# Kernel tuning notes

Measured on AMD Instinct MI355X. Metric: run time of the kernel, lower is better.

The kernel has to match this reference:

```python
import jax, jax.numpy as jnp
import numpy as np

B, T, HID = 1, 2048, 2048
H, KVH, D = 32, 8, 64
G = H // KVH          # kv groups = 4
SCALE = 1.0 / np.sqrt(D)
NEG = -1e9


def _rotate_half(x):
    x1, x2 = x[..., : D // 2], x[..., D // 2 :]
    return jnp.concatenate((-x2, x1), axis=-1)


def setup_inputs() -> dict:
    key = jax.random.key(0)
    ks = jax.random.split(key, 8)
    hidden_states = jax.random.normal(ks[0], (B, T, HID), jnp.float32)
    # RoPE tables (faithful shapes; realistic values)
    pos = jnp.arange(T, dtype=jnp.float32)[:, None]
    inv = 1.0 / (10000.0 ** (jnp.arange(0, D, 2, dtype=jnp.float32) / D))
    ang = pos * inv[None, :]                      # [T, D/2]
    ang = jnp.concatenate([ang, ang], axis=-1)    # [T, D]
    cos = jnp.broadcast_to(jnp.cos(ang)[None], (B, T, D))
    sin = jnp.broadcast_to(jnp.sin(ang)[None], (B, T, D))
    # causal additive mask [B,1,T,T]
    causal = jnp.tril(jnp.ones((T, T), bool))
    attention_mask_4d = jnp.where(causal, 0.0, NEG).astype(jnp.float32)[None, None]
    s = 0.02
    Wq = jax.random.normal(ks[1], (H * D, HID), jnp.float32) * s
    Wk = jax.random.normal(ks[2], (KVH * D, HID), jnp.float32) * s
    Wv = jax.random.normal(ks[3], (KVH * D, HID), jnp.float32) * s
    Wo = jax.random.normal(ks[4], (HID, H * D), jnp.float32) * s
    return {"hidden_states": hidden_states, "cos": cos, "sin": sin,
            "attention_mask_4d": attention_mask_4d,
            "Wq": Wq, "Wk": Wk, "Wv": Wv, "Wo": Wo}


def reference(hidden_states, cos, sin, attention_mask_4d, Wq, Wk, Wv, Wo):
    x = hidden_states
    b, t, _ = x.shape
    # QKV projections (nn.Linear: x @ W.T), then [B, heads, T, D]
    q = (x @ Wq.T).reshape(b, t, H, D).transpose(0, 2, 1, 3)
    k = (x @ Wk.T).reshape(b, t, KVH, D).transpose(0, 2, 1, 3)
    v = (x @ Wv.T).reshape(b, t, KVH, D).transpose(0, 2, 1, 3)
    # rotary: cos/sin [B,T,D] -> broadcast over heads
    c = cos[:, None]; s = sin[:, None]
    q = q * c + _rotate_half(q) * s
    k = k * c + _rotate_half(k) * s
    # grouped-query attention with fp32 scores/softmax
    qg = q.reshape(b, KVH, G, t, D)
    scores = jnp.einsum('bkgtd,bksd->bkgts', qg.astype(jnp.float32),
                        k.astype(jnp.float32)) * SCALE
    m = attention_mask_4d[:, 0].astype(jnp.float32)  # [B,T,S]
    scores = scores + m[:, None, None, :, :]
    probs = jax.nn.softmax(scores, axis=-1)
    out = jnp.einsum('bkgts,bksd->bkgtd', probs.astype(v.dtype), v)
    out = out.astype(q.dtype).reshape(b, H, t, D)
    out = out.transpose(0, 2, 1, 3).reshape(b, t, H * D)
    return out @ Wo.T
```

## Files before the change

### kernel.cpp

```cpp
#include <hip/hip_runtime.h>
#include <math.h>

typedef __attribute__((ext_vector_type(8))) __bf16 bf16x8;
typedef __attribute__((ext_vector_type(4))) float  f32x4;
typedef unsigned short ushort_t;
typedef unsigned int   uint_t;

static __device__ inline f32x4 mfma16(bf16x8 a, bf16x8 b, f32x4 c) {
    return __builtin_amdgcn_mfma_f32_16x16x32_bf16(a, b, c, 0, 0, 0);
}

static __device__ inline ushort_t f2b(float f) {
    uint_t u = __builtin_bit_cast(uint_t, f);
    u = (u + 0x7FFFu + ((u >> 16) & 1u)) >> 16;
    return (ushort_t)u;
}
static __device__ inline float b2f(ushort_t u) {
    uint_t x = ((uint_t)u) << 16;
    return __builtin_bit_cast(float, x);
}
static __device__ inline bf16x8 ld8(const ushort_t* p) {
    uint4 v = *(const uint4*)p;
    return __builtin_bit_cast(bf16x8, v);
}
static __device__ inline float fexp2(float x) {
#if __has_builtin(__builtin_amdgcn_exp2f)
    return __builtin_amdgcn_exp2f(x);
#else
    return exp2f(x);
#endif
}

static __device__ inline void gl_lds16(const ushort_t* g, ushort_t* l) {
    __builtin_amdgcn_global_load_lds(
        (const __attribute__((address_space(1))) void*)(g),
        (__attribute__((address_space(3))) void*)(l),
        16, 0, 0);
}

#define WS_XB     0
#define WS_WQKV   8388608
#define WS_WO     20971520
#define WS_P0     29360128
#define WS_P1     41943040
#define WS_QBB    0
#define WS_KBB    8388608
#define WS_VTG    10485760
#define WS_AB     12582912
#define WS_O0     29360128
#define WS_O1     46137344

__global__ __launch_bounds__(256) void cvt_all(const float* __restrict__ x,
                                               const float* __restrict__ wq,
                                               const float* __restrict__ wk,
                                               const float* __restrict__ wv,
                                               const float* __restrict__ wo,
                                               ushort_t* __restrict__ dst) {
    const size_t i = (size_t)(blockIdx.x * 256 + threadIdx.x) * 4;
    const float* src; size_t off;
    if (i < 4194304)       { src = x;  off = 0; }
    else if (i < 8388608)  { src = wq; off = 4194304; }
    else if (i < 9437184)  { src = wk; off = 8388608; }
    else if (i < 10485760) { src = wv; off = 9437184; }
    else                   { src = wo; off = 10485760; }
    float4 v = *(const float4*)(src + (i - off));
    ushort4 o;
    o.x = f2b(v.x); o.y = f2b(v.y); o.z = f2b(v.z); o.w = f2b(v.w);
    *(ushort4*)(dst + i) = o;
}

template <int OUTB>
__global__ __launch_bounds__(512, 2) void gemm256(const ushort_t* __restrict__ A,
                                                  const ushort_t* __restrict__ Bt,
                                                  void* __restrict__ C0,
                                                  void* __restrict__ C1,
                                                  int N, int K) {
    __shared__ ushort_t lds[65536];
    const int tid  = threadIdx.x;
    const int lane = tid & 63, w = tid >> 6;
    const int qn = lane & 15, quad = lane >> 4;
    const long m0 = (long)blockIdx.y * 256;
    const long n0 = (long)blockIdx.x * 256;
    const int kh   = K >> 1;
    const int kbeg = blockIdx.z * kh;
    const int NT   = kh >> 6;
    void* Cout = blockIdx.z ? C1 : C0;
    ushort_t* ldsp = lds;

    const int srow = w * 8 + (lane >> 3);
    const int scol = ((lane & 7) ^ (lane >> 3)) * 8;
    const ushort_t* gA = A  + (m0 + srow) * (size_t)K + kbeg + scol;
    const ushort_t* gB = Bt + (n0 + srow) * (size_t)K + kbeg + scol;

    const int aRow = ((w >> 2) * 64 + qn) * 64;
    const int bRow = ((w & 3) * 32 + qn) * 64;
    const int sw0 = ((quad * 16)      ^ ((qn & 7) << 4)) >> 1;
    const int sw1 = ((64 + quad * 16) ^ ((qn & 7) << 4)) >> 1;

#define STG_A(t, h, buf)                                                       \
    do { if ((t) < NT) {                                                       \
        const ushort_t* g = gA + (size_t)(h) * 128 * K + (t) * 64;             \
        ushort_t* d = ldsp + (buf) * 32768 + (h) * 8192 + w * 512;             \
        gl_lds16(g, d);                                                        \
        gl_lds16(g + 64 * (size_t)K, d + 4096);                                \
    } } while (0)
#define STG_B(t, h, buf)                                                       \
    do { if ((t) < NT) {                                                       \
        const ushort_t* g = gB + (size_t)(h) * 128 * K + (t) * 64;             \
        ushort_t* d = ldsp + (buf) * 32768 + 16384 + (h) * 8192 + w * 512;     \
        gl_lds16(g, d);                                                        \
        gl_lds16(g + 64 * (size_t)K, d + 4096);                                \
    } } while (0)

#define PHASE(cb, p, qr, qc, STAGE, BOUND)                                     \
    do {                                                                       \
        const ushort_t* bA = ldsp + (cb) * 32768 + (qr) * 8192;                \
        const ushort_t* bB = ldsp + (cb) * 32768 + 16384 + (qc) * 8192;        \
        bf16x8 af[4][2], bv[2][2];                                             \
        _Pragma("unroll")                                                      \
        for (int mi = 0; mi < 4; mi++) {                                       \
            af[mi][0] = *(const bf16x8*)(bA + aRow + mi * 1024 + sw0);         \
            af[mi][1] = *(const bf16x8*)(bA + aRow + mi * 1024 + sw1);         \
        }                                                                      \
        _Pragma("unroll")                                                      \
        for (int nj = 0; nj < 2; nj++) {                                       \
            bv[nj][0] = *(const bf16x8*)(bB + bRow + nj * 1024 + sw0);         \
            bv[nj][1] = *(const bf16x8*)(bB + bRow + nj * 1024 + sw1);         \
        }                                                                      \
        asm volatile("" ::: "memory");          \
        STAGE;                                                                 \
        BOUND;                                                                 \
        __builtin_amdgcn_s_barrier();                                          \
        asm volatile("s_waitcnt lgkmcnt(0)" ::: "memory");                     \
        __builtin_amdgcn_sched_barrier(0);                                     \
        __builtin_amdgcn_s_setprio(1);                                         \
        _Pragma("unroll")                                                      \
        for (int mi = 0; mi < 4; mi++)                                         \
            _Pragma("unroll")                                                  \
            for (int nj = 0; nj < 2; nj++) {                                   \
                acc[p][mi][nj] = mfma16(af[mi][0], bv[nj][0], acc[p][mi][nj]); \
                acc[p][mi][nj] = mfma16(af[mi][1], bv[nj][1], acc[p][mi][nj]); \
            }                                                                  \
        __builtin_amdgcn_s_setprio(0);                                         \
        __builtin_amdgcn_s_barrier();                                          \
    } while (0)

    f32x4 acc[4][4][2];
    f32x4 zero = {0.f, 0.f, 0.f, 0.f};
    #pragma unroll
    for (int p = 0; p < 4; p++)
        #pragma unroll
        for (int mi = 0; mi < 4; mi++)
            #pragma unroll
            for (int nj = 0; nj < 2; nj++) acc[p][mi][nj] = zero;

    STG_A(0, 0, 0); STG_B(0, 0, 0); STG_B(0, 1, 0); STG_A(0, 1, 0);
    STG_A(1, 0, 1); STG_B(1, 0, 1);
    asm volatile("s_waitcnt vmcnt(0)" ::: "memory");
    __builtin_amdgcn_s_barrier();

    for (int t2 = 0; t2 < NT; t2 += 2) {
        PHASE(0, 0, 0, 0, STG_B(t2 + 1, 1, 1), (void)0);
        PHASE(0, 1, 0, 1, STG_A(t2 + 1, 1, 1), (void)0);
        PHASE(0, 2, 1, 0, STG_A(t2 + 2, 0, 0), (void)0);
        PHASE(0, 3, 1, 1, STG_B(t2 + 2, 0, 0),
              if (t2 == NT - 2) { asm volatile("s_waitcnt vmcnt(0)" ::: "memory"); }
              else              { asm volatile("s_waitcnt vmcnt(4)" ::: "memory"); });
        PHASE(1, 0, 0, 0, STG_B(t2 + 2, 1, 0), (void)0);
        PHASE(1, 1, 0, 1, STG_A(t2 + 2, 1, 0), (void)0);
        PHASE(1, 2, 1, 0, STG_A(t2 + 3, 0, 1), (void)0);
        PHASE(1, 3, 1, 1, STG_B(t2 + 3, 0, 1),
              asm volatile("s_waitcnt vmcnt(4)" ::: "memory"););
    }
#undef PHASE
#undef STG_A
#undef STG_B

    #pragma unroll
    for (int p = 0; p < 4; p++) {
        const int qr = p >> 1, qc = p & 1;
        #pragma unroll
        for (int mi = 0; mi < 4; mi++)
            #pragma unroll
            for (int nj = 0; nj < 2; nj++) {
                const long row0 = m0 + qr * 128 + (w >> 2) * 64 + mi * 16 + quad * 4;
                const long col  = n0 + qc * 128 + (w & 3) * 32 + nj * 16 + qn;
                #pragma unroll
                for (int r = 0; r < 4; r++) {
                    if (OUTB)
                        ((ushort_t*)Cout)[(row0 + r) * N + col] = f2b(acc[p][mi][nj][r]);
                    else
                        ((float*)Cout)[(row0 + r) * N + col] = acc[p][mi][nj][r];
                }
            }
    }
}

__global__ __launch_bounds__(512, 2) void gemm_op(const ushort_t* __restrict__ A,
                                                  const ushort_t* __restrict__ Bt,
                                                  float* __restrict__ C0,
                                                  float* __restrict__ C1,
                                                  int N, int K) {
    __shared__ ushort_t lds[49152];
    const int tid  = threadIdx.x;
    const int lane = tid & 63, w = tid >> 6;
    const int qn = lane & 15, quad = lane >> 4;
    const long m0 = (long)blockIdx.y * 256;
    const long n0 = (long)blockIdx.x * 128;
    const int kh   = K >> 1;
    const int kbeg = blockIdx.z * kh;
    const int NT   = kh >> 6;
    float* Cout = blockIdx.z ? C1 : C0;
    ushort_t* ldsp = lds;

    const int srow = w * 8 + (lane >> 3);
    const int scol = ((lane & 7) ^ (lane >> 3)) * 8;
    const ushort_t* gA = A + (m0 + srow) * (size_t)K + kbeg + scol;
    const int srB  = tid >> 3;
    const int scB  = ((tid & 7) ^ (srB & 7)) * 8;
    const ushort_t* gB = Bt + (n0 + srB) * (size_t)K + kbeg + scB;

    const int wm = w >> 1, wn = w & 1;
    const int aRow = (wm * 32 + qn) * 64;
    const int bRow = (wn * 32 + qn) * 64;
    const int sw0 = ((quad * 16)      ^ ((qn & 7) << 4)) >> 1;
    const int sw1 = ((64 + quad * 16) ^ ((qn & 7) << 4)) >> 1;

#define OSTG_A(t, h, buf)                                                      \
    do { if ((t) < NT) {                                                       \
        const ushort_t* g = gA + (size_t)(h) * 128 * K + (t) * 64;             \
        ushort_t* d = ldsp + (buf) * 24576 + (h) * 8192 + w * 512;             \
        gl_lds16(g, d);                                                        \
        gl_lds16(g + 64 * (size_t)K, d + 4096);                                \
    } } while (0)
#define OSTG_B(t, h, buf)                                                      \
    do { if ((t) < NT) {                                                       \
        const ushort_t* g = gB + (size_t)(h) * 64 * K + (t) * 64;              \
        ushort_t* d = ldsp + (buf) * 24576 + 16384 + (h) * 4096 + w * 512;     \
        gl_lds16(g, d);                                                        \
    } } while (0)

#define OPHASE(cb, p, qr, qc, STAGE, BOUND)                                    \
    do {                                                                       \
        const ushort_t* bA = ldsp + (cb) * 24576 + (qr) * 8192;                \
        const ushort_t* bB = ldsp + (cb) * 24576 + 16384 + (qc) * 4096;        \
        bf16x8 af[2][2], bv[2][2];                                             \
        _Pragma("unroll")                                                      \
        for (int mi = 0; mi < 2; mi++) {                                       \
            af[mi][0] = *(const bf16x8*)(bA + aRow + mi * 1024 + sw0);         \
            af[mi][1] = *(const bf16x8*)(bA + aRow + mi * 1024 + sw1);         \
        }                                                                      \
        _Pragma("unroll")                                                      \
        for (int nj = 0; nj < 2; nj++) {                                       \
            bv[nj][0] = *(const bf16x8*)(bB + bRow + nj * 1024 + sw0);         \
            bv[nj][1] = *(const bf16x8*)(bB + bRow + nj * 1024 + sw1);         \
        }                                                                      \
        asm volatile("" ::: "memory");                                         \
        STAGE;                                                                 \
        BOUND;                                                                 \
        __builtin_amdgcn_s_barrier();                                          \
        asm volatile("s_waitcnt lgkmcnt(0)" ::: "memory");                     \
        __builtin_amdgcn_sched_barrier(0);                                     \
        __builtin_amdgcn_s_setprio(1);                                         \
        _Pragma("unroll")                                                      \
        for (int mi = 0; mi < 2; mi++)                                         \
            _Pragma("unroll")                                                  \
            for (int nj = 0; nj < 2; nj++) {                                   \
                acc[p][mi][nj] = mfma16(af[mi][0], bv[nj][0], acc[p][mi][nj]); \
                acc[p][mi][nj] = mfma16(af[mi][1], bv[nj][1], acc[p][mi][nj]); \
            }                                                                  \
        __builtin_amdgcn_s_setprio(0);                                         \
        __builtin_amdgcn_s_barrier();                                          \
    } while (0)

    f32x4 acc[4][2][2];
    f32x4 zero = {0.f, 0.f, 0.f, 0.f};
    #pragma unroll
    for (int p = 0; p < 4; p++)
        #pragma unroll
        for (int mi = 0; mi < 2; mi++)
            #pragma unroll
            for (int nj = 0; nj < 2; nj++) acc[p][mi][nj] = zero;

    OSTG_A(0, 0, 0); OSTG_B(0, 0, 0); OSTG_B(0, 1, 0); OSTG_A(0, 1, 0);
    OSTG_A(1, 0, 1); OSTG_B(1, 0, 1);
    asm volatile("s_waitcnt vmcnt(0)" ::: "memory");
    __builtin_amdgcn_s_barrier();

    for (int t2 = 0; t2 < NT; t2 += 2) {
        OPHASE(0, 0, 0, 0, OSTG_B(t2 + 1, 1, 1), (void)0);
        OPHASE(0, 1, 0, 1, OSTG_A(t2 + 1, 1, 1), (void)0);
        OPHASE(0, 2, 1, 0, OSTG_A(t2 + 2, 0, 0), (void)0);
        OPHASE(0, 3, 1, 1, OSTG_B(t2 + 2, 0, 0),
               if (t2 == NT - 2) { asm volatile("s_waitcnt vmcnt(0)" ::: "memory"); }
               else              { asm volatile("s_waitcnt vmcnt(3)" ::: "memory"); });
        OPHASE(1, 0, 0, 0, OSTG_B(t2 + 2, 1, 0), (void)0);
        OPHASE(1, 1, 0, 1, OSTG_A(t2 + 2, 1, 0), (void)0);
        OPHASE(1, 2, 1, 0, OSTG_A(t2 + 3, 0, 1), (void)0);
        OPHASE(1, 3, 1, 1, OSTG_B(t2 + 3, 0, 1),
               asm volatile("s_waitcnt vmcnt(3)" ::: "memory"););
    }
#undef OPHASE
#undef OSTG_A
#undef OSTG_B

    #pragma unroll
    for (int p = 0; p < 4; p++) {
        const int qr = p >> 1, qc = p & 1;
        #pragma unroll
        for (int mi = 0; mi < 2; mi++)
            #pragma unroll
            for (int nj = 0; nj < 2; nj++) {
                const long row0 = m0 + qr * 128 + wm * 32 + mi * 16 + quad * 4;
                const long col  = n0 + qc * 64 + wn * 32 + nj * 16 + qn;
                #pragma unroll
                for (int r = 0; r < 4; r++)
                    Cout[(row0 + r) * N + col] = acc[p][mi][nj][r];
            }
    }
}

__global__ __launch_bounds__(256) void fuse_crv(const ushort_t* __restrict__ p0,
                                                const ushort_t* __restrict__ p1,
                                                const float* __restrict__ cs,
                                                const float* __restrict__ sn,
                                                ushort_t* __restrict__ qd,
                                                ushort_t* __restrict__ kd,
                                                ushort_t* __restrict__ vt) {
    __shared__ ushort_t tl[64][65];
    const int cx = blockIdx.x;
    const int ty = blockIdx.y;
    const int r  = threadIdx.x >> 2;
    const int c0 = (threadIdx.x & 3) << 4;
    const int t  = ty * 64 + r;
    const size_t base = (size_t)t * 3072 + cx * 64;

    if (cx < 40) {
        const int cp = c0 ^ 32;
        float own[16], par[16];
        #pragma unroll
        for (int jj = 0; jj < 2; jj++) {
            uint4 a = *(const uint4*)(p0 + base + c0 + jj * 8);
            uint4 b = *(const uint4*)(p1 + base + c0 + jj * 8);
            uint4 c = *(const uint4*)(p0 + base + cp + jj * 8);
            uint4 d = *(const uint4*)(p1 + base + cp + jj * 8);
            const ushort_t* pa = (const ushort_t*)&a;
            const ushort_t* pb = (const ushort_t*)&b;
            const ushort_t* pc = (const ushort_t*)&c;
            const ushort_t* pd = (const ushort_t*)&d;
            #pragma unroll
            for (int e = 0; e < 8; e++) {
                own[jj * 8 + e] = b2f(pa[e]) + b2f(pb[e]);
                par[jj * 8 + e] = b2f(pc[e]) + b2f(pd[e]);
            }
        }
        float cs16[16], sn16[16];
        #pragma unroll
        for (int jj = 0; jj < 4; jj++) {
            float4 c4 = *(const float4*)(cs + (size_t)t * 64 + c0 + jj * 4);
            float4 s4 = *(const float4*)(sn + (size_t)t * 64 + c0 + jj * 4);
            cs16[jj * 4 + 0] = c4.x; cs16[jj * 4 + 1] = c4.y;
            cs16[jj * 4 + 2] = c4.z; cs16[jj * 4 + 3] = c4.w;
            sn16[jj * 4 + 0] = s4.x; sn16[jj * 4 + 1] = s4.y;
            sn16[jj * 4 + 2] = s4.z; sn16[jj * 4 + 3] = s4.w;
        }
        const float scale = (cx < 32) ? 0.18033688f : 1.0f;
        union { ushort_t u[16]; uint4 v[2]; } o;
        #pragma unroll
        for (int j = 0; j < 16; j++) {
            const int d = c0 + j;
            const float pr = (d < 32) ? -par[j] : par[j];
            o.u[j] = f2b((own[j] * cs16[j] + pr * sn16[j]) * scale);
        }
        if (cx < 32) {
            ushort_t* dst = qd + (size_t)t * 2048 + cx * 64 + c0;
            *(uint4*)dst = o.v[0]; *(uint4*)(dst + 8) = o.v[1];
        } else {
            ushort_t* dst = kd + (size_t)t * 512 + (cx - 32) * 64 + c0;
            *(uint4*)dst = o.v[0]; *(uint4*)(dst + 8) = o.v[1];
        }
    } else {
        #pragma unroll
        for (int jj = 0; jj < 2; jj++) {
            uint4 a = *(const uint4*)(p0 + base + c0 + jj * 8);
            uint4 b = *(const uint4*)(p1 + base + c0 + jj * 8);
            const ushort_t* pa = (const ushort_t*)&a;
            const ushort_t* pb = (const ushort_t*)&b;
            #pragma unroll
            for (int e = 0; e < 8; e++)
                tl[r][c0 + jj * 8 + e] = f2b(b2f(pa[e]) + b2f(pb[e]));
        }
        __syncthreads();
        const int rr  = threadIdx.x >> 3;
        const int cc8 = (threadIdx.x & 7) * 8;
        const int db = (cx - 40) * 64, tb = ty * 64;
        #pragma unroll
        for (int h = 0; h < 2; h++) {
            const int d = rr + h * 32;
            ushort4 o0, o1;
            o0.x = tl[cc8 + 0][d]; o0.y = tl[cc8 + 1][d];
            o0.z = tl[cc8 + 2][d]; o0.w = tl[cc8 + 3][d];
            o1.x = tl[cc8 + 4][d]; o1.y = tl[cc8 + 5][d];
            o1.z = tl[cc8 + 6][d]; o1.w = tl[cc8 + 7][d];
            *(ushort4*)(vt + (size_t)(db + d) * 2048 + tb + cc8)     = o0;
            *(ushort4*)(vt + (size_t)(db + d) * 2048 + tb + cc8 + 4) = o1;
        }
    }
}

__global__ __launch_bounds__(256) void combine_o(const float4* __restrict__ s0,
                                                 const float4* __restrict__ s1,
                                                 float4* __restrict__ out) {
    for (int i = blockIdx.x * 256 + threadIdx.x; i < 1048576; i += 2048 * 256) {
        float4 a = s0[i], b = s1[i];
        float4 r; r.x = a.x + b.x; r.y = a.y + b.y; r.z = a.z + b.z; r.w = a.w + b.w;
        out[i] = r;
    }
}

__global__ __launch_bounds__(256) void attn_kernel(const ushort_t* __restrict__ Q,
                                                   const ushort_t* __restrict__ Kb,
                                                   const ushort_t* __restrict__ Vt,
                                                   ushort_t* __restrict__ Ob) {
    __shared__ ushort_t Ks[2 * 4096];
    __shared__ ushort_t Vs[2 * 4096];
    __shared__ ushort_t pl[4 * 16 * 72];
    const int tid  = threadIdx.x;
    const int lane = tid & 63, wid = tid >> 6;
    const int qn = lane & 15, quad = lane >> 4;
    const int h   = blockIdx.x & 31;
    const int qb  = 31 - (blockIdx.x >> 5);
    const int kvb = (h >> 2) * 64;
    const int trow = qb * 64 + wid * 16;
    ushort_t* plw = pl + wid * 16 * 72;
    f32x4 zero = {0.f, 0.f, 0.f, 0.f};

    const ushort_t* qpA = Q + (size_t)(trow + qn) * 2048 + h * 64 + quad * 8;
    const bf16x8 qA0 = ld8(qpA), qA1 = ld8(qpA + 32);

    f32x4 oA[4] = {zero, zero, zero, zero};
    float lA[4] = {0.f, 0.f, 0.f, 0.f};
    const int ntiles = qb + 1;

#define STAGE(s0, buf)                                                         \
    do {                                                                       \
        const ushort_t* kg = Kb + (size_t)((s0) + lane) * 512 + kvb + wid * 8; \
        gl_lds16(kg,      Ks + (buf) * 4096 + wid * 512);                      \
        gl_lds16(kg + 32, Ks + (buf) * 4096 + (wid + 4) * 512);                \
        const ushort_t* vg = Vt + (size_t)(kvb + lane) * 2048 + (s0) + wid * 8;\
        gl_lds16(vg,      Vs + (buf) * 4096 + wid * 512);                      \
        gl_lds16(vg + 32, Vs + (buf) * 4096 + (wid + 4) * 512);                \
    } while (0)

#define COMPUTE(s0, buf)                                                       \
    do {                                                                       \
        f32x4 scA[4];                                                          \
        __builtin_amdgcn_s_setprio(1);                                         \
        _Pragma("unroll")                                                      \
        for (int cb = 0; cb < 4; cb++) {                                       \
            const bf16x8 kf0 = *(const bf16x8*)(Ks + (buf) * 4096 + quad * 512 + (cb * 16 + qn) * 8);       \
            const bf16x8 kf1 = *(const bf16x8*)(Ks + (buf) * 4096 + (quad + 4) * 512 + (cb * 16 + qn) * 8); \
            f32x4 s = mfma16(qA0, kf0, zero); scA[cb] = mfma16(qA1, kf1, s);   \
        }                                                                      \
        __builtin_amdgcn_s_setprio(0);                                         \
        const bool needmask = ((s0) + 63 > trow);                              \
        _Pragma("unroll")                                                      \
        for (int i = 0; i < 4; i++) {                                          \
            const int tA = trow + quad * 4 + i;                                \
            _Pragma("unroll")                                                  \
            for (int cb = 0; cb < 4; cb++) {                                   \
                const int col = (s0) + cb * 16 + qn;                           \
                float vA = scA[cb][i];                                         \
                if (needmask) {                                                \
                    if (col > tA) vA = -INFINITY;                              \
                }                                                              \
                const float pA = fexp2(vA);                                    \
                lA[i] += pA;                                                   \
                plw[(quad * 4 + i) * 72 + cb * 16 + qn] = f2b(pA);             \
            }                                                                  \
        }                                                                      \
        const bf16x8 pfA0 = *(const bf16x8*)(plw + qn * 72 + quad * 8);        \
        const bf16x8 pfA1 = *(const bf16x8*)(plw + qn * 72 + 32 + quad * 8);   \
        __builtin_amdgcn_s_setprio(1);                                         \
        _Pragma("unroll")                                                      \
        for (int dcb = 0; dcb < 4; dcb++) {                                    \
            const bf16x8 vf0 = *(const bf16x8*)(Vs + (buf) * 4096 + quad * 512 + (dcb * 16 + qn) * 8);       \
            const bf16x8 vf1 = *(const bf16x8*)(Vs + (buf) * 4096 + (quad + 4) * 512 + (dcb * 16 + qn) * 8); \
            oA[dcb] = mfma16(pfA0, vf0, oA[dcb]);                              \
            oA[dcb] = mfma16(pfA1, vf1, oA[dcb]);                              \
        }                                                                      \
        __builtin_amdgcn_s_setprio(0);                                         \
    } while (0)

    STAGE(0, 0);
    int t = 0;
    for (; t + 2 <= ntiles; t += 2) {
        __syncthreads();
        STAGE((t + 1) * 64, 1);
        COMPUTE(t * 64, 0);
        __syncthreads();
        if (t + 2 < ntiles) STAGE((t + 2) * 64, 0);
        COMPUTE((t + 1) * 64, 1);
    }
    if (t < ntiles) {
        __syncthreads();
        COMPUTE(t * 64, 0);
    }
#undef STAGE
#undef COMPUTE

    #pragma unroll
    for (int i = 0; i < 4; i++) {
        float sA = lA[i];
        #pragma unroll
        for (int off = 1; off < 16; off <<= 1)
            sA += __shfl_xor(sA, off, 64);
        const float invA = 1.0f / sA;
        ushort_t* obA = Ob + (size_t)(trow + quad * 4 + i) * 2048 + h * 64 + qn;
        obA[0]  = f2b(oA[0][i] * invA);
        obA[16] = f2b(oA[1][i] * invA);
        obA[32] = f2b(oA[2][i] * invA);
        obA[48] = f2b(oA[3][i] * invA);
    }
}

extern "C" void kernel_launch(void* const* d_in, const int* in_sizes, int n_in,
                              void* d_out, int out_size, void* d_ws, size_t ws_size,
                              hipStream_t stream) {
    const float* x    = (const float*)d_in[0];
    const float* cosp = (const float*)d_in[1];
    const float* sinp = (const float*)d_in[2];
    const float* Wq = (const float*)d_in[4];
    const float* Wk = (const float*)d_in[5];
    const float* Wv = (const float*)d_in[6];
    const float* Wo = (const float*)d_in[7];
    char* ws = (char*)d_ws;
    (void)ws_size; (void)in_sizes; (void)n_in; (void)out_size;

    ushort_t* xb    = (ushort_t*)(ws + WS_XB);
    ushort_t* wqkvb = (ushort_t*)(ws + WS_WQKV);
    ushort_t* wob   = (ushort_t*)(ws + WS_WO);
    ushort_t* p0    = (ushort_t*)(ws + WS_P0);
    ushort_t* p1    = (ushort_t*)(ws + WS_P1);
    ushort_t* qbb   = (ushort_t*)(ws + WS_QBB);
    ushort_t* kbb   = (ushort_t*)(ws + WS_KBB);
    ushort_t* vtg   = (ushort_t*)(ws + WS_VTG);
    ushort_t* ab    = (ushort_t*)(ws + WS_AB);
    float*    o0    = (float*)   (ws + WS_O0);
    float*    o1    = (float*)   (ws + WS_O1);

    cvt_all<<<14336, 256, 0, stream>>>(x, Wq, Wk, Wv, Wo, xb);

    gemm256<1><<<dim3(12, 8, 2), 512, 0, stream>>>(xb, wqkvb, p0, p1, 3072, 2048);

    fuse_crv<<<dim3(48, 32), 256, 0, stream>>>(p0, p1, cosp, sinp, qbb, kbb, vtg);

    attn_kernel<<<1024, 256, 0, stream>>>(qbb, kbb, vtg, ab);

    gemm_op<<<dim3(16, 8, 2), 512, 0, stream>>>(ab, wob, o0, o1, 2048, 2048);

    combine_o<<<2048, 256, 0, stream>>>((const float4*)o0, (const float4*)o1,
                                        (float4*)d_out);
}
```

Before: 250.8 us.

## Replace split-K output projection with 256x64 tile GEMM writing output directly

The output projection GEMM no longer splits K in two and then sums the partial fp32 outputs in a separate combine kernel. It now uses 256x64 output tiles over the full K range, with 256 blocks and a 2-stage pipeline, and stores straight to the output. This removes a kernel launch and the write and re-read of two 16MB partial buffers. In exchange each block's K loop is twice as long, per-block reuse of the A tile is lower, and there is less work per phase to hide load latency.

```diff
diff --git a/kernel.cpp b/kernel.cpp
--- a/kernel.cpp
+++ b/kernel.cpp
@@ -47,8 +47,6 @@
 #define WS_KBB    8388608
 #define WS_VTG    10485760
 #define WS_AB     12582912
-#define WS_O0     29360128
-#define WS_O1     46137344
 
 __global__ __launch_bounds__(256) void cvt_all(const float* __restrict__ x,
                                                const float* __restrict__ wq,
@@ -196,29 +194,25 @@
     }
 }
 
-__global__ __launch_bounds__(512, 2) void gemm_op(const ushort_t* __restrict__ A,
+__global__ __launch_bounds__(512, 2) void gemm_on(const ushort_t* __restrict__ A,
                                                   const ushort_t* __restrict__ Bt,
-                                                  float* __restrict__ C0,
-                                                  float* __restrict__ C1,
+                                                  float* __restrict__ Cout,
                                                   int N, int K) {
-    __shared__ ushort_t lds[49152];
+    __shared__ ushort_t lds[40960];
     const int tid  = threadIdx.x;
     const int lane = tid & 63, w = tid >> 6;
     const int qn = lane & 15, quad = lane >> 4;
     const long m0 = (long)blockIdx.y * 256;
-    const long n0 = (long)blockIdx.x * 128;
-    const int kh   = K >> 1;
-    const int kbeg = blockIdx.z * kh;
-    const int NT   = kh >> 6;
-    float* Cout = blockIdx.z ? C1 : C0;
+    const long n0 = (long)blockIdx.x * 64;
+    const int NT = K >> 6;
     ushort_t* ldsp = lds;
 
     const int srow = w * 8 + (lane >> 3);
     const int scol = ((lane & 7) ^ (lane >> 3)) * 8;
-    const ushort_t* gA = A + (m0 + srow) * (size_t)K + kbeg + scol;
+    const ushort_t* gA = A + (m0 + srow) * (size_t)K + scol;
     const int srB  = tid >> 3;
     const int scB  = ((tid & 7) ^ (srB & 7)) * 8;
-    const ushort_t* gB = Bt + (n0 + srB) * (size_t)K + kbeg + scB;
+    const ushort_t* gB = Bt + (n0 + srB) * (size_t)K + scB;
 
     const int wm = w >> 1, wn = w & 1;
     const int aRow = (wm * 32 + qn) * 64;
@@ -226,24 +220,24 @@
     const int sw0 = ((quad * 16)      ^ ((qn & 7) << 4)) >> 1;
     const int sw1 = ((64 + quad * 16) ^ ((qn & 7) << 4)) >> 1;
 
-#define OSTG_A(t, h, buf)                                                      \
+#define NSTG_A(t, h, buf)                                                      \
     do { if ((t) < NT) {                                                       \
         const ushort_t* g = gA + (size_t)(h) * 128 * K + (t) * 64;             \
-        ushort_t* d = ldsp + (buf) * 24576 + (h) * 8192 + w * 512;             \
+        ushort_t* d = ldsp + (buf) * 20480 + (h) * 8192 + w * 512;             \
         gl_lds16(g, d);                                                        \
         gl_lds16(g + 64 * (size_t)K, d + 4096);                                \
     } } while (0)
-#define OSTG_B(t, h, buf)                                                      \
+#define NSTG_B(t, buf)                                                         \
     do { if ((t) < NT) {                                                       \
-        const ushort_t* g = gB + (size_t)(h) * 64 * K + (t) * 64;              \
-        ushort_t* d = ldsp + (buf) * 24576 + 16384 + (h) * 4096 + w * 512;     \
+        const ushort_t* g = gB + (size_t)(t) * 64;                             \
+        ushort_t* d = ldsp + (buf) * 20480 + 16384 + w * 512;                  \
         gl_lds16(g, d);                                                        \
     } } while (0)
 
-#define OPHASE(cb, p, qr, qc, STAGE, BOUND)                                    \
+#define NPHASE(cb, qr, STAGE, BOUND)                                           \
     do {                                                                       \
-        const ushort_t* bA = ldsp + (cb) * 24576 + (qr) * 8192;                \
-        const ushort_t* bB = ldsp + (cb) * 24576 + 16384 + (qc) * 4096;        \
+        const ushort_t* bA = ldsp + (cb) * 20480 + (qr) * 8192;                \
+        const ushort_t* bB = ldsp + (cb) * 20480 + 16384;                      \
         bf16x8 af[2][2], bv[2][2];                                             \
         _Pragma("unroll")                                                      \
         for (int mi = 0; mi < 2; mi++) {                                       \
@@ -266,58 +260,51 @@
         for (int mi = 0; mi < 2; mi++)                                         \
             _Pragma("unroll")                                                  \
             for (int nj = 0; nj < 2; nj++) {                                   \
-                acc[p][mi][nj] = mfma16(af[mi][0], bv[nj][0], acc[p][mi][nj]); \
-                acc[p][mi][nj] = mfma16(af[mi][1], bv[nj][1], acc[p][mi][nj]); \
+                acc[qr][mi][nj] = mfma16(af[mi][0], bv[nj][0], acc[qr][mi][nj]); \
+                acc[qr][mi][nj] = mfma16(af[mi][1], bv[nj][1], acc[qr][mi][nj]); \
             }                                                                  \
         __builtin_amdgcn_s_setprio(0);                                         \
         __builtin_amdgcn_s_barrier();                                          \
     } while (0)
 
-    f32x4 acc[4][2][2];
+    f32x4 acc[2][2][2];
     f32x4 zero = {0.f, 0.f, 0.f, 0.f};
     #pragma unroll
-    for (int p = 0; p < 4; p++)
+    for (int p = 0; p < 2; p++)
         #pragma unroll
         for (int mi = 0; mi < 2; mi++)
             #pragma unroll
             for (int nj = 0; nj < 2; nj++) acc[p][mi][nj] = zero;
 
-    OSTG_A(0, 0, 0); OSTG_B(0, 0, 0); OSTG_B(0, 1, 0); OSTG_A(0, 1, 0);
-    OSTG_A(1, 0, 1); OSTG_B(1, 0, 1);
+    NSTG_A(0, 0, 0); NSTG_A(0, 1, 0); NSTG_B(0, 0);
+    NSTG_A(1, 0, 1);
     asm volatile("s_waitcnt vmcnt(0)" ::: "memory");
     __builtin_amdgcn_s_barrier();
 
-    for (int t2 = 0; t2 < NT; t2 += 2) {
-        OPHASE(0, 0, 0, 0, OSTG_B(t2 + 1, 1, 1), (void)0);
-        OPHASE(0, 1, 0, 1, OSTG_A(t2 + 1, 1, 1), (void)0);
-        OPHASE(0, 2, 1, 0, OSTG_A(t2 + 2, 0, 0), (void)0);
-        OPHASE(0, 3, 1, 1, OSTG_B(t2 + 2, 0, 0),
-               if (t2 == NT - 2) { asm volatile("s_waitcnt vmcnt(0)" ::: "memory"); }
-               else              { asm volatile("s_waitcnt vmcnt(3)" ::: "memory"); });
-        OPHASE(1, 0, 0, 0, OSTG_B(t2 + 2, 1, 0), (void)0);
-        OPHASE(1, 1, 0, 1, OSTG_A(t2 + 2, 1, 0), (void)0);
-        OPHASE(1, 2, 1, 0, OSTG_A(t2 + 3, 0, 1), (void)0);
-        OPHASE(1, 3, 1, 1, OSTG_B(t2 + 3, 0, 1),
-               asm volatile("s_waitcnt vmcnt(3)" ::: "memory"););
-    }
-#undef OPHASE
-#undef OSTG_A
-#undef OSTG_B
+    for (int t = 0; t < NT; t++) {
+        const int cb = t & 1;
+        NPHASE(cb, 0, { NSTG_A(t + 1, 1, cb ^ 1); NSTG_B(t + 1, cb ^ 1); },
+               (void)0);
+        NPHASE(cb, 1, { NSTG_A(t + 2, 0, cb); },
+               if (t == NT - 2) { asm volatile("s_waitcnt vmcnt(0)" ::: "memory"); }
+               else             { asm volatile("s_waitcnt vmcnt(2)" ::: "memory"); });
+    }
+#undef NPHASE
+#undef NSTG_A
+#undef NSTG_B
 
     #pragma unroll
-    for (int p = 0; p < 4; p++) {
-        const int qr = p >> 1, qc = p & 1;
+    for (int p = 0; p < 2; p++)
         #pragma unroll
         for (int mi = 0; mi < 2; mi++)
             #pragma unroll
             for (int nj = 0; nj < 2; nj++) {
-                const long row0 = m0 + qr * 128 + wm * 32 + mi * 16 + quad * 4;
-                const long col  = n0 + qc * 64 + wn * 32 + nj * 16 + qn;
+                const long row0 = m0 + p * 128 + wm * 32 + mi * 16 + quad * 4;
+                const long col  = n0 + wn * 32 + nj * 16 + qn;
                 #pragma unroll
                 for (int r = 0; r < 4; r++)
                     Cout[(row0 + r) * N + col] = acc[p][mi][nj][r];
             }
-    }
 }
 
 __global__ __launch_bounds__(256) void fuse_crv(const ushort_t* __restrict__ p0,
@@ -408,16 +395,6 @@
     }
 }
 
-__global__ __launch_bounds__(256) void combine_o(const float4* __restrict__ s0,
-                                                 const float4* __restrict__ s1,
-                                                 float4* __restrict__ out) {
-    for (int i = blockIdx.x * 256 + threadIdx.x; i < 1048576; i += 2048 * 256) {
-        float4 a = s0[i], b = s1[i];
-        float4 r; r.x = a.x + b.x; r.y = a.y + b.y; r.z = a.z + b.z; r.w = a.w + b.w;
-        out[i] = r;
-    }
-}
-
 __global__ __launch_bounds__(256) void attn_kernel(const ushort_t* __restrict__ Q,
                                                    const ushort_t* __restrict__ Kb,
                                                    const ushort_t* __restrict__ Vt,
@@ -546,8 +523,6 @@
     ushort_t* kbb   = (ushort_t*)(ws + WS_KBB);
     ushort_t* vtg   = (ushort_t*)(ws + WS_VTG);
     ushort_t* ab    = (ushort_t*)(ws + WS_AB);
-    float*    o0    = (float*)   (ws + WS_O0);
-    float*    o1    = (float*)   (ws + WS_O1);
 
     cvt_all<<<14336, 256, 0, stream>>>(x, Wq, Wk, Wv, Wo, xb);
 
@@ -557,8 +532,5 @@
 
     attn_kernel<<<1024, 256, 0, stream>>>(qbb, kbb, vtg, ab);
 
-    gemm_op<<<dim3(16, 8, 2), 512, 0, stream>>>(ab, wob, o0, o1, 2048, 2048);
-
-    combine_o<<<2048, 256, 0, stream>>>((const float4*)o0, (const float4*)o1,
-                                        (float4*)d_out);
-}
+    gemm_on<<<dim3(32, 8), 512, 0, stream>>>(ab, wob, (float*)d_out, 2048, 2048);
+}
```

New measurement: 243.0 us. 1.03x faster.
